# Performance work log

Hardware: AMD Instinct MI355X
Metric: run time of the kernel (lower is better)

Reference implementation:

```python
import jax, jax.numpy as jnp
import numpy as np

T, B, D, H, NQ = 512, 64, 256, 512, 64

def _uniform(key, shape, fan_in):
    b = 1.0 / np.sqrt(fan_in)
    return jax.random.uniform(key, shape, jnp.float32, -b, b)

def setup_inputs() -> dict:
    key = jax.random.key(0)
    ks = jax.random.split(key, 17)
    inp = {"x": jax.random.normal(ks[0], (T, B, D), jnp.float32)}
    fan1 = D + H
    names = ["f", "i", "g", "o"]
    for j, n in enumerate(names):
        inp[f"W{n}"] = _uniform(ks[1 + 2 * j], (fan1, NQ), fan1)
        inp[f"b{n}"] = _uniform(ks[2 + 2 * j], (NQ,), fan1)
    for j, n in enumerate(names):
        inp[f"M{n}"] = _uniform(ks[9 + 2 * j], (NQ, H), NQ)
        inp[f"mb{n}"] = _uniform(ks[10 + 2 * j], (H,), NQ)
    return inp

def reference(x, Wf, bf, Wi, bi, Wg, bg, Wo, bo, Mf, mbf, Mi, mbi, Mg, mbg, Mo, mbo):
    Bsz = x.shape[1]
    h0 = jnp.zeros((Bsz, H), x.dtype)
    c0 = jnp.zeros((Bsz, H), x.dtype)

    def step(carry, xt):
        h, c = carry
        combined = jnp.concatenate([xt, h], axis=1)  # [B, D+H]
        f = jax.nn.sigmoid((combined @ Wf + bf) @ Mf + mbf)
        i = jax.nn.sigmoid((combined @ Wi + bi) @ Mi + mbi)
        g = jnp.tanh((combined @ Wg + bg) @ Mg + mbg)
        o = jax.nn.sigmoid((combined @ Wo + bo) @ Mo + mbo)
        c = f * c + i * g
        h = o * jnp.tanh(c)
        return (h, c), h

    (hT, cT), stacked = jax.lax.scan(step, (h0, c0), x)
    return stacked, hT, cT
```

## Files before the change

### kernel.cpp

```cpp
#include <hip/hip_runtime.h>
#include <hip/hip_bf16.h>


#define NBLK 32
#define SENT16 ((short)0x7FC0)

typedef __attribute__((ext_vector_type(8))) short s16x8;
typedef __attribute__((ext_vector_type(4))) float f32x4;

static __device__ __forceinline__ unsigned short f2bf(float f) {
    union { float f; unsigned int u; } v; v.f = f;
    return (unsigned short)((v.u + 0x7FFFu + ((v.u >> 16) & 1u)) >> 16);
}
static __device__ __forceinline__ float sigmoid_f(float x) {
    x = fminf(fmaxf(x, -30.f), 30.f);
    float e = __expf(-x);
    return __builtin_amdgcn_rcpf(1.f + e);
}
static __device__ __forceinline__ float tanh_f(float x) {
    x = fminf(fmaxf(x, -15.f), 15.f);
    float e = __expf(2.f * x);
    return 1.f - 2.f * __builtin_amdgcn_rcpf(1.f + e);
}

__global__ __launch_bounds__(256) void prep_kernel(
    const float* __restrict__ x,
    const float* __restrict__ Wf, const float* __restrict__ bf_,
    const float* __restrict__ Wi, const float* __restrict__ bi_,
    const float* __restrict__ Wg, const float* __restrict__ bg_,
    const float* __restrict__ Wo, const float* __restrict__ bo_,
    const float* __restrict__ Mf, const float* __restrict__ mbf_,
    const float* __restrict__ Mi, const float* __restrict__ mbi_,
    const float* __restrict__ Mg, const float* __restrict__ mbg_,
    const float* __restrict__ Mo, const float* __restrict__ mbo_,
    unsigned short* __restrict__ Khp,
    unsigned short* __restrict__ Kxp,
    float* __restrict__ bias_out,
    unsigned short* __restrict__ xbf,
    unsigned short* __restrict__ hb)
{
    const float* Ws[4] = {Wf, Wi, Wg, Wo};
    const float* Ms[4] = {Mf, Mi, Mg, Mo};
    const float* bs[4] = {bf_, bi_, bg_, bo_};
    const float* mbs[4] = {mbf_, mbi_, mbg_, mbo_};
    const long long NKH = 512LL * 2048;
    const long long NKX = 256LL * 2048;
    const long long NB_ = 2048;
    const long long NX = 512LL * 64 * 256;
    const long long NHB = 4LL * 32768;
    const long long total = NKH + NKX + NB_ + NX + NHB;
    for (long long id = (long long)blockIdx.x * blockDim.x + threadIdx.x; id < total;
         id += (long long)gridDim.x * blockDim.x) {
        if (id < NKH) {
            int i = (int)id;
            int k = i >> 11, scol = i & 2047;
            int n = scol >> 9, c = scol & 511;
            const float* W = Ws[n]; const float* M = Ms[n];
            float acc = 0.f;
            #pragma unroll 8
            for (int q = 0; q < 64; ++q) acc = fmaf(W[(256 + k) * 64 + q], M[q * 512 + c], acc);
            int blk = c >> 4, jj = c & 15, kc = k >> 5;
            int l = (((k >> 3) & 3) << 4) | jj, j = k & 7;
            Khp[((((blk * 4 + n) * 16 + kc) * 64 + l) << 3) + j] = f2bf(acc);
        } else if (id < NKH + NKX) {
            int i = (int)(id - NKH);
            int k = i >> 11, scol = i & 2047;
            int n = scol >> 9, c = scol & 511;
            const float* W = Ws[n]; const float* M = Ms[n];
            float acc = 0.f;
            #pragma unroll 8
            for (int q = 0; q < 64; ++q) acc = fmaf(W[k * 64 + q], M[q * 512 + c], acc);
            int blk = c >> 4, jj = c & 15, kc = k >> 5;
            int l = (((k >> 3) & 3) << 4) | jj, j = k & 7;
            Kxp[((((blk * 4 + n) * 8 + kc) * 64 + l) << 3) + j] = f2bf(acc);
        } else if (id < NKH + NKX + NB_) {
            int scol = (int)(id - NKH - NKX);
            int n = scol >> 9, c = scol & 511;
            const float* M = Ms[n];
            float acc = mbs[n][c];
            #pragma unroll 8
            for (int q = 0; q < 64; ++q) acc = fmaf(bs[n][q], M[q * 512 + c], acc);
            bias_out[scol] = acc;
        } else if (id < NKH + NKX + NB_ + NX) {
            long long e = id - NKH - NKX - NB_;
            xbf[e] = f2bf(x[e]);
        } else {
            int e = (int)(id - NKH - NKX - NB_ - NX);
            hb[e] = (e < 32768) ? (unsigned short)0 : (unsigned short)0x7FC0;
        }
    }
}

#define HLOAD(i, off_) \
    asm volatile("global_load_dwordx4 %0, %1, off offset:" #off_ " sc0 sc1" \
                 : "=&v"(hfrag[i]) : "v"(hr))

__global__ __launch_bounds__(64, 1) void qlstm_persist(
    const unsigned short* __restrict__ xbf,
    const unsigned short* __restrict__ Khp,
    const unsigned short* __restrict__ Kxp,
    const float* __restrict__ bias,
    float* __restrict__ out,
    unsigned short* hbuf)
{
    extern __shared__ unsigned short smem[];
    unsigned short* lKh = smem;
    unsigned short* lKx = smem + 32768;
    const int tid = threadIdx.x;
    const int slot = blockIdx.x & 31, w = blockIdx.x >> 5;
    const int lane = tid;

    {
        const uint4* src = (const uint4*)(Khp + (size_t)slot * 32768);
        uint4* dst = (uint4*)lKh;
        for (int i = tid; i < 4096; i += 64) dst[i] = src[i];
        const uint4* src2 = (const uint4*)(Kxp + (size_t)slot * 16384);
        uint4* dst2 = (uint4*)lKx;
        for (int i = tid; i < 2048; i += 64) dst2[i] = src2[i];
    }
    __syncthreads();

    const int jj = lane & 15, lhi = lane >> 4;
    const int hcol = slot * 16 + jj;
    const int row0 = w * 16;
    const int browbase = row0 + lhi * 4;

    float bias_v[4];
    #pragma unroll
    for (int n = 0; n < 4; ++n) bias_v[n] = bias[n * 512 + hcol];
    float c_state[4] = {0.f, 0.f, 0.f, 0.f};

    s16x8 xfrag[8];
    {
        const unsigned short* xr = xbf + (long long)(row0 + jj) * 256 + lhi * 8;
        #pragma unroll
        for (int kc = 0; kc < 8; ++kc) xfrag[kc] = *(const s16x8*)(xr + kc * 32);
    }

    for (int t = 0; t < 512; ++t) {
        const unsigned short* hcur = hbuf + (t & 3) * 32768;
        unsigned short* hnext = hbuf + ((t + 1) & 3) * 32768;
        unsigned short* hpois = hbuf + ((t + 3) & 3) * 32768;

        f32x4 acc[4];
        #pragma unroll
        for (int n = 0; n < 4; ++n) {
            f32x4 b0 = {bias_v[n], bias_v[n], bias_v[n], bias_v[n]};
            acc[n] = b0;
        }
        #pragma unroll
        for (int kc = 0; kc < 8; ++kc) {
            #pragma unroll
            for (int n = 0; n < 4; ++n) {
                s16x8 b = *(const s16x8*)(lKx + (((n * 8 + kc) * 64 + lane) << 3));
                acc[n] = __builtin_amdgcn_mfma_f32_16x16x32_bf16(xfrag[kc], b, acc[n], 0, 0, 0);
            }
        }

        s16x8 hfrag[16];
        const unsigned short* hr = hcur + (row0 + jj) * 512 + lhi * 8;
        int sweeps = 0;
        for (;;) {
            HLOAD(0, 0);    HLOAD(1, 64);   HLOAD(2, 128);  HLOAD(3, 192);
            HLOAD(4, 256);  HLOAD(5, 320);  HLOAD(6, 384);  HLOAD(7, 448);
            HLOAD(8, 512);  HLOAD(9, 576);  HLOAD(10, 640); HLOAD(11, 704);
            HLOAD(12, 768); HLOAD(13, 832); HLOAD(14, 896); HLOAD(15, 960);
            asm volatile("s_waitcnt vmcnt(0)" ::: "memory");
            __builtin_amdgcn_sched_barrier(0);
            int bad = 0;
            #pragma unroll
            for (int kc = 0; kc < 16; ++kc)
                bad |= (hfrag[kc][0] == SENT16) | (hfrag[kc][4] == SENT16);
            if (!__any(bad) || ++sweeps > 16384) break;
        }
        __builtin_amdgcn_sched_barrier(0);

        if (t < 511) {
            const unsigned short* xr = xbf + ((long long)(t + 1) * 64 + row0 + jj) * 256 + lhi * 8;
            #pragma unroll
            for (int kc = 0; kc < 8; ++kc) xfrag[kc] = *(const s16x8*)(xr + kc * 32);
        }
        {
            unsigned long long s64 = 0x7FC07FC07FC07FC0ull;
            unsigned long long* pa = (unsigned long long*)
                (hpois + (row0 + (lane >> 2)) * 512 + slot * 16 + (lane & 3) * 4);
            asm volatile("global_store_dwordx2 %0, %1, off sc0 sc1"
                         :: "v"(pa), "v"(s64) : "memory");
        }

        #pragma unroll
        for (int kc = 0; kc < 16; ++kc) {
            #pragma unroll
            for (int n = 0; n < 4; ++n) {
                s16x8 b = *(const s16x8*)(lKh + (((n * 16 + kc) * 64 + lane) << 3));
                acc[n] = __builtin_amdgcn_mfma_f32_16x16x32_bf16(hfrag[kc], b, acc[n], 0, 0, 0);
            }
        }

        float hv[4], cv[4];
        #pragma unroll
        for (int r = 0; r < 4; ++r) {
            float fv = sigmoid_f(acc[0][r]);
            float iv = sigmoid_f(acc[1][r]);
            float gv = tanh_f(acc[2][r]);
            float ov = sigmoid_f(acc[3][r]);
            float c = fmaf(fv, c_state[r], iv * gv);
            c_state[r] = c;
            float h = ov * tanh_f(c);
            hv[r] = h; cv[r] = c;
            unsigned int myb = f2bf(h);
            unsigned int o1 = (unsigned int)__shfl_xor((int)myb, 1, 64);
            unsigned int b01 = (myb & 0xFFFFu) | (o1 << 16);
            unsigned long long o2 =
                (unsigned long long)(unsigned int)__shfl_xor((int)b01, 2, 64);
            unsigned long long q = (unsigned long long)b01 | (o2 << 32);
            if ((jj & 3) == 0) {
                unsigned long long* ha =
                    (unsigned long long*)(hnext + (browbase + r) * 512 + slot * 16 + jj);
                asm volatile("global_store_dwordx2 %0, %1, off sc0 sc1"
                             :: "v"(ha), "v"(q) : "memory");
            }
        }

        float* outt = out + (long long)t * 32768;
        #pragma unroll
        for (int r = 0; r < 4; ++r) {
            const int brow = browbase + r;
            outt[brow * 512 + hcol] = hv[r];
            if (t == 511) {
                out[16777216 + brow * 512 + hcol] = hv[r];
                out[16809984 + brow * 512 + hcol] = cv[r];
            }
        }
    }
}

extern "C" void kernel_launch(void* const* d_in, const int* in_sizes, int n_in,
                              void* d_out, int out_size, void* d_ws, size_t ws_size,
                              hipStream_t stream) {
    const float* x   = (const float*)d_in[0];
    const float* Wf  = (const float*)d_in[1];  const float* bf_  = (const float*)d_in[2];
    const float* Wi  = (const float*)d_in[3];  const float* bi_  = (const float*)d_in[4];
    const float* Wg  = (const float*)d_in[5];  const float* bg_  = (const float*)d_in[6];
    const float* Wo  = (const float*)d_in[7];  const float* bo_  = (const float*)d_in[8];
    const float* Mf  = (const float*)d_in[9];  const float* mbf_ = (const float*)d_in[10];
    const float* Mi  = (const float*)d_in[11]; const float* mbi_ = (const float*)d_in[12];
    const float* Mg  = (const float*)d_in[13]; const float* mbg_ = (const float*)d_in[14];
    const float* Mo  = (const float*)d_in[15]; const float* mbo_ = (const float*)d_in[16];
    float* outp = (float*)d_out;

    char* ws = (char*)d_ws;
    unsigned short* xbf  = (unsigned short*)(ws);
    unsigned short* Khp  = (unsigned short*)(ws + 16777216);
    unsigned short* Kxp  = (unsigned short*)(ws + 18874368);
    float*          bias = (float*)        (ws + 19922944);
    unsigned short* hbuf = (unsigned short*)(ws + 19931136);
    if (ws_size < 20193280) return;

    prep_kernel<<<4096, 256, 0, stream>>>(
        x, Wf, bf_, Wi, bi_, Wg, bg_, Wo, bo_,
        Mf, mbf_, Mi, mbi_, Mg, mbg_, Mo, mbo_,
        Khp, Kxp, bias, xbf, hbuf);

    hipFuncSetAttribute((const void*)qlstm_persist,
                        hipFuncAttributeMaxDynamicSharedMemorySize, 98304);

    const unsigned short* xbf_c = xbf;
    const unsigned short* Khp_c = Khp;
    const unsigned short* Kxp_c = Kxp;
    const float* bias_c = bias;
    float* out_c = outp;
    unsigned short* hbuf_c = hbuf;
    void* args[] = {(void*)&xbf_c, (void*)&Khp_c, (void*)&Kxp_c, (void*)&bias_c,
                    (void*)&out_c, (void*)&hbuf_c};
    hipLaunchCooperativeKernel((const void*)qlstm_persist, dim3(128), dim3(64),
                               args, 98304, stream);
}
```

Measured before the change: 1.891 ms.

## Replace sentinel-polled hidden-state handoff with per-group atomic step counters

Drops the NaN-sentinel scheme, in which each block re-read the whole hidden-state slice until no poisoned values remained and poisoned a future buffer every step. Each row group now has a counter that blocks atomically increment after their h stores complete, and readers spin on that counter before a single load of h. Because the counter orders reads against later overwrites, the hidden-state ring shrinks from four buffers to two. The aim is to remove the poison stores, the repeated full-slice polling and the sentinel checks. In exchange, each step adds a serial counter round-trip before the h loads and an extra store wait before the atomic.

Result: slower. 2.284 ms (+20.8%).

```diff
diff --git a/kernel.cpp b/kernel.cpp
--- a/kernel.cpp
+++ b/kernel.cpp
@@ -3,7 +3,6 @@
 
 
 #define NBLK 32
-#define SENT16 ((short)0x7FC0)
 
 typedef __attribute__((ext_vector_type(8))) short s16x8;
 typedef __attribute__((ext_vector_type(4))) float f32x4;
@@ -47,7 +46,7 @@
     const long long NKX = 256LL * 2048;
     const long long NB_ = 2048;
     const long long NX = 512LL * 64 * 256;
-    const long long NHB = 4LL * 32768;
+    const long long NHB = 2LL * 32768;
     const long long total = NKH + NKX + NB_ + NX + NHB;
     for (long long id = (long long)blockIdx.x * blockDim.x + threadIdx.x; id < total;
          id += (long long)gridDim.x * blockDim.x) {
@@ -86,7 +85,7 @@
             xbf[e] = f2bf(x[e]);
         } else {
             int e = (int)(id - NKH - NKX - NB_ - NX);
-            hb[e] = (e < 32768) ? (unsigned short)0 : (unsigned short)0x7FC0;
+            hb[e] = (unsigned short)0;
         }
     }
 }
@@ -101,7 +100,8 @@
     const unsigned short* __restrict__ Kxp,
     const float* __restrict__ bias,
     float* __restrict__ out,
-    unsigned short* hbuf)
+    unsigned short* hbuf,
+    unsigned int* ctr)
 {
     extern __shared__ unsigned short smem[];
     unsigned short* lKh = smem;
@@ -124,6 +124,7 @@
     const int hcol = slot * 16 + jj;
     const int row0 = w * 16;
     const int browbase = row0 + lhi * 4;
+    unsigned int* myctr = ctr + w * 64;
 
     float bias_v[4];
     #pragma unroll
@@ -138,9 +139,8 @@
     }
 
     for (int t = 0; t < 512; ++t) {
-        const unsigned short* hcur = hbuf + (t & 3) * 32768;
-        unsigned short* hnext = hbuf + ((t + 1) & 3) * 32768;
-        unsigned short* hpois = hbuf + ((t + 3) & 3) * 32768;
+        const unsigned short* hcur = hbuf + (t & 1) * 32768;
+        unsigned short* hnext = hbuf + ((t + 1) & 1) * 32768;
 
         f32x4 acc[4];
         #pragma unroll
@@ -157,36 +157,34 @@
             }
         }
 
+        {
+            const unsigned int tgt = (unsigned)t * NBLK;
+            int guard = 0;
+            for (;;) {
+                unsigned cv_;
+                asm volatile("global_load_dword %0, %1, off sc0 sc1\n\t"
+                             "s_waitcnt vmcnt(0)"
+                             : "=v"(cv_) : "v"(myctr) : "memory");
+                if (cv_ >= tgt || ++guard > 20000) break;
+            }
+        }
+        __builtin_amdgcn_sched_barrier(0);
+
         s16x8 hfrag[16];
         const unsigned short* hr = hcur + (row0 + jj) * 512 + lhi * 8;
-        int sweeps = 0;
-        for (;;) {
-            HLOAD(0, 0);    HLOAD(1, 64);   HLOAD(2, 128);  HLOAD(3, 192);
-            HLOAD(4, 256);  HLOAD(5, 320);  HLOAD(6, 384);  HLOAD(7, 448);
-            HLOAD(8, 512);  HLOAD(9, 576);  HLOAD(10, 640); HLOAD(11, 704);
-            HLOAD(12, 768); HLOAD(13, 832); HLOAD(14, 896); HLOAD(15, 960);
-            asm volatile("s_waitcnt vmcnt(0)" ::: "memory");
-            __builtin_amdgcn_sched_barrier(0);
-            int bad = 0;
-            #pragma unroll
-            for (int kc = 0; kc < 16; ++kc)
-                bad |= (hfrag[kc][0] == SENT16) | (hfrag[kc][4] == SENT16);
-            if (!__any(bad) || ++sweeps > 16384) break;
-        }
-        __builtin_amdgcn_sched_barrier(0);
+        HLOAD(0, 0);    HLOAD(1, 64);   HLOAD(2, 128);  HLOAD(3, 192);
+        HLOAD(4, 256);  HLOAD(5, 320);  HLOAD(6, 384);  HLOAD(7, 448);
+        HLOAD(8, 512);  HLOAD(9, 576);  HLOAD(10, 640); HLOAD(11, 704);
+        HLOAD(12, 768); HLOAD(13, 832); HLOAD(14, 896); HLOAD(15, 960);
 
         if (t < 511) {
             const unsigned short* xr = xbf + ((long long)(t + 1) * 64 + row0 + jj) * 256 + lhi * 8;
             #pragma unroll
             for (int kc = 0; kc < 8; ++kc) xfrag[kc] = *(const s16x8*)(xr + kc * 32);
         }
-        {
-            unsigned long long s64 = 0x7FC07FC07FC07FC0ull;
-            unsigned long long* pa = (unsigned long long*)
-                (hpois + (row0 + (lane >> 2)) * 512 + slot * 16 + (lane & 3) * 4);
-            asm volatile("global_store_dwordx2 %0, %1, off sc0 sc1"
-                         :: "v"(pa), "v"(s64) : "memory");
-        }
+
+        asm volatile("s_waitcnt vmcnt(0)" ::: "memory");
+        __builtin_amdgcn_sched_barrier(0);
 
         #pragma unroll
         for (int kc = 0; kc < 16; ++kc) {
@@ -222,6 +220,10 @@
             }
         }
 
+        asm volatile("s_waitcnt vmcnt(0)" ::: "memory");
+        __builtin_amdgcn_sched_barrier(0);
+        if (tid == 0) atomicAdd(myctr, 1u);
+
         float* outt = out + (long long)t * 32768;
         #pragma unroll
         for (int r = 0; r < 4; ++r) {
@@ -255,7 +257,10 @@
     unsigned short* Kxp  = (unsigned short*)(ws + 18874368);
     float*          bias = (float*)        (ws + 19922944);
     unsigned short* hbuf = (unsigned short*)(ws + 19931136);
-    if (ws_size < 20193280) return;
+    unsigned int*   ctr  = (unsigned int*) (ws + 20062208);
+    if (ws_size < 20063232) return;
+
+    hipMemsetAsync(ctr, 0, 1024, stream);
 
     prep_kernel<<<4096, 256, 0, stream>>>(
         x, Wf, bf_, Wi, bi_, Wg, bg_, Wo, bo_,
@@ -271,8 +276,9 @@
     const float* bias_c = bias;
     float* out_c = outp;
     unsigned short* hbuf_c = hbuf;
+    unsigned int* ctr_c = ctr;
     void* args[] = {(void*)&xbf_c, (void*)&Khp_c, (void*)&Kxp_c, (void*)&bias_c,
-                    (void*)&out_c, (void*)&hbuf_c};
+                    (void*)&out_c, (void*)&hbuf_c, (void*)&ctr_c};
     hipLaunchCooperativeKernel((const void*)qlstm_persist, dim3(128), dim3(64),
                                args, 98304, stream);
 }
```
